# Performance work log

Hardware: AMD Instinct MI355X
Metric: run time of the kernel (lower is better)

Reference implementation:

```python
import jax, jax.numpy as jnp
import numpy as np

D = 1024
H = 16
DK = D // H
HID = 4096
EPS = 1e-5


def setup_inputs() -> dict:
    key = jax.random.key(0)
    ks = jax.random.split(key, 16)
    B, S = 2, 2048
    sc = lambda fan_in: 1.0 / np.sqrt(fan_in)
    inp = {
        "x": jax.random.normal(ks[0], (B, S, D), jnp.float32),
        "y": jax.random.normal(ks[1], (B, S, D), jnp.float32),
        "mask": jnp.ones((B, 1, 1, S), jnp.int32),
        # attention projections, stored [in, out]
        "Wq": jax.random.normal(ks[2], (D, D), jnp.float32) * sc(D),
        "bq": jnp.zeros((D,), jnp.float32),
        "Wk": jax.random.normal(ks[3], (D, D), jnp.float32) * sc(D),
        "bk": jnp.zeros((D,), jnp.float32),
        "Wv": jax.random.normal(ks[4], (D, D), jnp.float32) * sc(D),
        "bv": jnp.zeros((D,), jnp.float32),
        "Wo": jax.random.normal(ks[5], (D, D), jnp.float32) * sc(D),
        "bo": jnp.zeros((D,), jnp.float32),
        # FFN
        "W1": jax.random.normal(ks[6], (D, HID), jnp.float32) * sc(D),
        "b1": jnp.zeros((HID,), jnp.float32),
        "W2": jax.random.normal(ks[7], (HID, D), jnp.float32) * sc(HID),
        "b2": jnp.zeros((D,), jnp.float32),
        # LayerNorms
        "g1": jnp.ones((D,), jnp.float32),
        "be1": jnp.zeros((D,), jnp.float32),
        "g2": jnp.ones((D,), jnp.float32),
        "be2": jnp.zeros((D,), jnp.float32),
    }
    return inp


def _layer_norm(x, g, b):
    m = jnp.mean(x, axis=-1, keepdims=True)
    v = jnp.mean(jnp.square(x - m), axis=-1, keepdims=True)
    return (x - m) * jax.lax.rsqrt(v + EPS) * g + b


def _split_heads(t):  # [B,S,D] -> [B,H,S,DK]
    B, S, _ = t.shape
    return t.reshape(B, S, H, DK).transpose(0, 2, 1, 3)


def reference(x, y, mask, Wq, bq, Wk, bk, Wv, bv, Wo, bo,
              W1, b1, W2, b2, g1, be1, g2, be2):
    scale = 1.0 / np.sqrt(DK)
    Q = _split_heads(x @ Wq + bq)
    K = _split_heads(y @ Wk + bk)
    V = _split_heads(y @ Wv + bv)
    scores = jnp.einsum("bhqd,bhkd->bhqk", Q, K) * scale  # [B,H,S,S]
    scores = jnp.where(mask == 0, jnp.float32(-1e9), scores)
    probs = jax.nn.softmax(scores, axis=-1)
    attn = jnp.einsum("bhqk,bhkd->bhqd", probs, V)
    B, _, S, _ = attn.shape
    attn = attn.transpose(0, 2, 1, 3).reshape(B, S, D)
    mha_out = attn @ Wo + bo
    x1 = _layer_norm(x + mha_out, g1, be1)
    ff = jax.nn.relu(x1 @ W1 + b1) @ W2 + b2
    return _layer_norm(x1 + ff, g2, be2)
```

## Files before the change

### kernel.cpp

```cpp
#include <hip/hip_runtime.h>

#define S_ 2048
#define D_ 1024
#define B_ 2
#define H_ 16
#define DK_ 64
#define HID_ 4096

typedef unsigned short u16;
typedef __attribute__((ext_vector_type(8))) short short8;
typedef __attribute__((ext_vector_type(4))) float f32x4;

__device__ __forceinline__ float bf2f(u16 u) {
  return __uint_as_float(((unsigned int)u) << 16);
}
__device__ __forceinline__ u16 f2bf(float f) {
  unsigned int x = __float_as_uint(f);
  x += 0x7fff + ((x >> 16) & 1);
  return (u16)(x >> 16);
}
__device__ __forceinline__ unsigned int pk2bf(float lo, float hi) {
  return ((__float_as_uint(lo) + 0x8000u) >> 16) | ((__float_as_uint(hi) + 0x8000u) & 0xffff0000u);
}

__global__ __launch_bounds__(256) void cvt_f2b(const float* __restrict__ in, u16* __restrict__ outp) {
  const int i = blockIdx.x * 256 + threadIdx.x;
  float4 v = ((const float4*)in)[i];
  unsigned int lo = (unsigned int)f2bf(v.x) | ((unsigned int)f2bf(v.y) << 16);
  unsigned int hi = (unsigned int)f2bf(v.z) | ((unsigned int)f2bf(v.w) << 16);
  ((uint2*)outp)[i] = make_uint2(lo, hi);
}

__global__ __launch_bounds__(256) void maskbias_k(const int* __restrict__ mask, float* __restrict__ biasf) {
  const int i = blockIdx.x * 256 + threadIdx.x;
  biasf[i] = mask[i] ? 0.f : -1e30f;
}

template<int MT, int NT, int OUTF32>
__global__ __launch_bounds__(256) void gemm_bt(
    const u16* __restrict__ A, const u16* __restrict__ Bt,
    const float* __restrict__ bias, void* __restrict__ Cv,
    int K, int lda, int ldb, int ldc,
    long sA, long sB, long sC, int relu) {
  constexpr int BM = MT * 32;
  constexpr int BN = NT * 32;
  __shared__ __align__(16) u16 As[BM * 32];
  __shared__ __align__(16) u16 Bs[BN * 32];
  const int z = blockIdx.z;
  A  += (long)z * sA;
  Bt += (long)z * sB;
  const int tid  = threadIdx.x;
  const int lane = tid & 63, wave = tid >> 6;
  const int quad = lane >> 4, l15 = lane & 15;
  const int wm = wave >> 1, wn = wave & 1;
  const u16* Ab = A  + (long)(blockIdx.y * BM) * lda;
  const u16* Bb = Bt + (long)(blockIdx.x * BN) * ldb;

  f32x4 acc[MT][NT];
#pragma unroll
  for (int i = 0; i < MT; ++i)
#pragma unroll
    for (int j = 0; j < NT; ++j) acc[i][j] = (f32x4){0.f, 0.f, 0.f, 0.f};

  const int r0  = tid >> 2;
  const int kk0 = (tid & 3) * 8;

  for (int kt = 0; kt < K; kt += 32) {
#pragma unroll
    for (int p = 0; p < BM / 64; ++p) {
      __builtin_amdgcn_global_load_lds(
          (const __attribute__((address_space(1))) void*)(Ab + (long)(p * 64 + r0) * lda + kt + kk0),
          (__attribute__((address_space(3))) void*)(&As[p * 2048 + tid * 8]), 16, 0, 0);
    }
#pragma unroll
    for (int p = 0; p < BN / 64; ++p) {
      __builtin_amdgcn_global_load_lds(
          (const __attribute__((address_space(1))) void*)(Bb + (long)(p * 64 + r0) * ldb + kt + kk0),
          (__attribute__((address_space(3))) void*)(&Bs[p * 2048 + tid * 8]), 16, 0, 0);
    }
    __syncthreads();
    short8 af[MT], bfr[NT];
#pragma unroll
    for (int mt = 0; mt < MT; ++mt)
      af[mt] = *(const short8*)&As[(wm * (MT * 16) + mt * 16 + l15) * 32 + quad * 8];
#pragma unroll
    for (int nt = 0; nt < NT; ++nt)
      bfr[nt] = *(const short8*)&Bs[(wn * (NT * 16) + nt * 16 + l15) * 32 + quad * 8];
#pragma unroll
    for (int mt = 0; mt < MT; ++mt)
#pragma unroll
      for (int nt = 0; nt < NT; ++nt)
        acc[mt][nt] = __builtin_amdgcn_mfma_f32_16x16x32_bf16(af[mt], bfr[nt], acc[mt][nt], 0, 0, 0);
    __syncthreads();
  }

#pragma unroll
  for (int nt = 0; nt < NT; ++nt) {
    const int col = blockIdx.x * BN + wn * (NT * 16) + nt * 16 + l15;
    const float bvv = bias ? bias[col] : 0.f;
#pragma unroll
    for (int mt = 0; mt < MT; ++mt) {
#pragma unroll
      for (int r = 0; r < 4; ++r) {
        const int row = blockIdx.y * BM + wm * (MT * 16) + mt * 16 + quad * 4 + r;
        float v = acc[mt][nt][r] + bvv;
        if (relu) v = fmaxf(v, 0.f);
        if (OUTF32) ((float*)Cv)[(long)z * sC + (long)row * ldc + col] = v;
        else        ((u16*)Cv)[(long)z * sC + (long)row * ldc + col] = f2bf(v);
      }
    }
  }
}

__global__ __launch_bounds__(256) void qkv_k(
    const u16* __restrict__ xb, const u16* __restrict__ yb,
    const u16* __restrict__ WqT, const u16* __restrict__ WkT, const u16* __restrict__ WvT,
    const float* __restrict__ bq, const float* __restrict__ bk, const float* __restrict__ bv,
    u16* __restrict__ Q, u16* __restrict__ Kp, u16* __restrict__ Vp) {
  __shared__ __align__(16) u16 As[128 * 32];
  __shared__ __align__(16) u16 Bs[128 * 32];
  const int z = blockIdx.z;
  const u16* A  = (z == 0) ? xb : yb;
  const u16* Bt = (z == 0) ? WqT : (z == 1) ? WkT : WvT;
  const float* bias = (z == 0) ? bq : (z == 1) ? bk : bv;
  u16* C = (z == 0) ? Q : (z == 1) ? Kp : Vp;
  const float sc = (z == 0) ? 0.18033688011112042f : 1.0f;
  const int tid  = threadIdx.x;
  const int lane = tid & 63, wave = tid >> 6;
  const int quad = lane >> 4, l15 = lane & 15;
  const int wm = wave >> 1, wn = wave & 1;
  const u16* Ab = A  + (long)(blockIdx.y * 128) * D_;
  const u16* Bb = Bt + (long)(blockIdx.x * 128) * D_;

  f32x4 acc[4][4];
#pragma unroll
  for (int i = 0; i < 4; ++i)
#pragma unroll
    for (int j = 0; j < 4; ++j) acc[i][j] = (f32x4){0.f, 0.f, 0.f, 0.f};

  const int r0  = tid >> 2;
  const int kk0 = (tid & 3) * 8;

  for (int kt = 0; kt < D_; kt += 32) {
#pragma unroll
    for (int p = 0; p < 2; ++p) {
      __builtin_amdgcn_global_load_lds(
          (const __attribute__((address_space(1))) void*)(Ab + (long)(p * 64 + r0) * D_ + kt + kk0),
          (__attribute__((address_space(3))) void*)(&As[p * 2048 + tid * 8]), 16, 0, 0);
      __builtin_amdgcn_global_load_lds(
          (const __attribute__((address_space(1))) void*)(Bb + (long)(p * 64 + r0) * D_ + kt + kk0),
          (__attribute__((address_space(3))) void*)(&Bs[p * 2048 + tid * 8]), 16, 0, 0);
    }
    __syncthreads();
    short8 af[4], bfr[4];
#pragma unroll
    for (int mt = 0; mt < 4; ++mt)
      af[mt] = *(const short8*)&As[(wm * 64 + mt * 16 + l15) * 32 + quad * 8];
#pragma unroll
    for (int nt = 0; nt < 4; ++nt)
      bfr[nt] = *(const short8*)&Bs[(wn * 64 + nt * 16 + l15) * 32 + quad * 8];
#pragma unroll
    for (int mt = 0; mt < 4; ++mt)
#pragma unroll
      for (int nt = 0; nt < 4; ++nt)
        acc[mt][nt] = __builtin_amdgcn_mfma_f32_16x16x32_bf16(af[mt], bfr[nt], acc[mt][nt], 0, 0, 0);
    __syncthreads();
  }

#pragma unroll
  for (int nt = 0; nt < 4; ++nt) {
    const int col = blockIdx.x * 128 + wn * 64 + nt * 16 + l15;
    const float bvv = bias[col];
#pragma unroll
    for (int mt = 0; mt < 4; ++mt) {
#pragma unroll
      for (int r = 0; r < 4; ++r) {
        const int row = blockIdx.y * 128 + wm * 64 + mt * 16 + quad * 4 + r;
        C[(long)row * D_ + col] = f2bf((acc[mt][nt][r] + bvv) * sc);
      }
    }
  }
}

__global__ void transpose_k(const float* __restrict__ in, u16* __restrict__ outp, int R, int Ccols) {
  __shared__ u16 tile[32][33];
  const int c0 = blockIdx.x * 32, r0 = blockIdx.y * 32;
  const int tx = threadIdx.x, ty = threadIdx.y;
  for (int i = ty; i < 32; i += 8)
    tile[i][tx] = f2bf(in[(long)(r0 + i) * Ccols + c0 + tx]);
  __syncthreads();
  for (int i = ty; i < 32; i += 8)
    outp[(long)(c0 + i) * R + r0 + tx] = tile[tx][i];
}

__global__ void vtrans_k(const u16* __restrict__ V, u16* __restrict__ Vt) {
  __shared__ u16 tile[32][33];
  const int bh = blockIdx.z, b = bh >> 4, h = bh & 15;
  const u16* in = V + (long)b * S_ * D_ + h * DK_;
  u16* outp = Vt + (long)bh * DK_ * S_;
  const int s0 = blockIdx.x * 32, d0 = blockIdx.y * 32;
  const int tx = threadIdx.x, ty = threadIdx.y;
  for (int i = ty; i < 32; i += 8)
    tile[i][tx] = in[(long)(s0 + i) * D_ + d0 + tx];
  __syncthreads();
  for (int i = ty; i < 32; i += 8)
    outp[(long)(d0 + i) * S_ + s0 + tx] = tile[tx][i];
}

#define FA_LDS 65536
__global__ __launch_bounds__(256, 2) void flash_k(
    const u16* __restrict__ Q, const u16* __restrict__ Kp, const u16* __restrict__ Vt,
    const float* __restrict__ biasf, u16* __restrict__ ctx) {
  extern __shared__ __align__(16) char smem[];
  u16* sQ = (u16*)smem;
  u16* sK = (u16*)(smem + 32768);
  u16* sV = (u16*)(smem + 40960);
  u16* sP = (u16*)(smem + 49152);

  const int bh = blockIdx.x, qt = blockIdx.y;
  const int b = bh >> 4, h = bh & 15;
  const int tid = threadIdx.x;
  const int w = tid >> 6, lane = tid & 63;
  const int quad = lane >> 4, l15 = lane & 15;
  const int swz = ((l15 ^ (l15 >> 2)) & 3) << 3;

  const u16* Qg  = Q  + ((long)b * S_ + qt * 256) * D_ + h * DK_;
  const u16* Kg  = Kp + (long)b * S_ * D_ + h * DK_;
  const u16* Vtg = Vt + (long)bh * DK_ * S_;
  const float* biasg = biasf + b * S_;
  u16* ctxg = ctx + ((long)b * S_ + qt * 256) * D_ + h * DK_;

  const int krow = tid >> 3, kc = tid & 7;
  const u16* kptr = Kg + (long)krow * D_ + kc * 8;
  const int ksw = ((kc >> 2) << 10) + krow * 32 + (kc & 3) * 8;
  const int vrow = tid >> 2, vc = tid & 3;
  const u16* vptr = Vtg + (long)vrow * S_ + vc * 8;
  const int vsw = vrow * 32 + vc * 8;

  uint4 kreg = *(const uint4*)kptr;
  uint4 vreg = *(const uint4*)vptr;

#pragma unroll
  for (int p = 0; p < 8; ++p) {
    const int idx = p * 256 + tid;
    const int row = idx >> 3, cb = idx & 7;
    uint4 v = *(const uint4*)(Qg + (long)row * D_ + cb * 8);
    *(uint4*)&sQ[(cb >> 2) * 8192 + row * 32 + (cb & 3) * 8] = v;
  }
  *(uint4*)&sK[ksw] = kreg;
  *(uint4*)&sV[vsw] = vreg;
  kreg = *(const uint4*)(kptr + 32 * D_);
  vreg = *(const uint4*)(vptr + 32);
  kptr += 64 * D_;
  vptr += 64;
  __syncthreads();

  short8 qf[4][2];
#pragma unroll
  for (int nt = 0; nt < 4; ++nt)
#pragma unroll
    for (int kt = 0; kt < 2; ++kt)
      qf[nt][kt] = *(const short8*)&sQ[kt * 8192 + (w * 64 + nt * 16 + l15) * 32 + quad * 8];

  float lsum[4] = {0.f, 0.f, 0.f, 0.f};
  f32x4 accO[4][4];
#pragma unroll
  for (int i = 0; i < 4; ++i)
#pragma unroll
    for (int j = 0; j < 4; ++j) accO[i][j] = (f32x4){0.f, 0.f, 0.f, 0.f};

  for (int t = 0; t < 64; ++t) {
    if (t) __syncthreads();
    const int buf = (t & 1) << 11;
    const int nbuf = buf ^ 2048;
    if (t < 63) {
      *(uint4*)&sK[nbuf + ksw] = kreg;
      *(uint4*)&sV[nbuf + vsw] = vreg;
      if (t < 62) {
        kreg = *(const uint4*)kptr;
        vreg = *(const uint4*)vptr;
        kptr += 32 * D_;
        vptr += 32;
      }
    }
    float4 bv0 = *(const float4*)(biasg + t * 32 + quad * 4);
    float4 bv1 = *(const float4*)(biasg + t * 32 + 16 + quad * 4);

    f32x4 accS[2][4];
#pragma unroll
    for (int i = 0; i < 2; ++i)
#pragma unroll
      for (int j = 0; j < 4; ++j) accS[i][j] = (f32x4){0.f, 0.f, 0.f, 0.f};
#pragma unroll
    for (int kt = 0; kt < 2; ++kt) {
      short8 kf0 = *(const short8*)&sK[buf + kt * 1024 + l15 * 32 + quad * 8];
      short8 kf1 = *(const short8*)&sK[buf + kt * 1024 + (16 + l15) * 32 + quad * 8];
#pragma unroll
      for (int nt = 0; nt < 4; ++nt) {
        accS[0][nt] = __builtin_amdgcn_mfma_f32_16x16x32_bf16(kf0, qf[nt][kt], accS[0][nt], 0, 0, 0);
        accS[1][nt] = __builtin_amdgcn_mfma_f32_16x16x32_bf16(kf1, qf[nt][kt], accS[1][nt], 0, 0, 0);
      }
    }
#pragma unroll
    for (int mt = 0; mt < 2; ++mt) {
      const float4 bv = mt ? bv1 : bv0;
      const int kvl = ((mt * 16 + quad * 4) ^ swz);
#pragma unroll
      for (int nt = 0; nt < 4; ++nt) {
        float p0 = exp2f(fminf(accS[mt][nt][0] + bv.x, 30.f));
        float p1 = exp2f(fminf(accS[mt][nt][1] + bv.y, 30.f));
        float p2 = exp2f(fminf(accS[mt][nt][2] + bv.z, 30.f));
        float p3 = exp2f(fminf(accS[mt][nt][3] + bv.w, 30.f));
        lsum[nt] += (p0 + p1) + (p2 + p3);
        *(uint2*)&sP[(w * 64 + nt * 16 + l15) * 32 + kvl] =
            make_uint2(pk2bf(p0, p1), pk2bf(p2, p3));
      }
    }
    short8 pf[4], vf[4];
#pragma unroll
    for (int m = 0; m < 4; ++m)
      pf[m] = *(const short8*)&sP[(w * 64 + m * 16 + l15) * 32 + ((quad * 8) ^ swz)];
#pragma unroll
    for (int n = 0; n < 4; ++n)
      vf[n] = *(const short8*)&sV[buf + (n * 16 + l15) * 32 + quad * 8];
#pragma unroll
    for (int m = 0; m < 4; ++m)
#pragma unroll
      for (int n = 0; n < 4; ++n)
        accO[m][n] = __builtin_amdgcn_mfma_f32_16x16x32_bf16(pf[m], vf[n], accO[m][n], 0, 0, 0);
  }

#pragma unroll
  for (int nt = 0; nt < 4; ++nt) {
    lsum[nt] += __shfl_xor(lsum[nt], 16, 64);
    lsum[nt] += __shfl_xor(lsum[nt], 32, 64);
  }
#pragma unroll
  for (int m = 0; m < 4; ++m) {
    float inv[4];
#pragma unroll
    for (int r = 0; r < 4; ++r)
      inv[r] = 1.f / __shfl(lsum[m], quad * 4 + r, 64);
#pragma unroll
    for (int n = 0; n < 4; ++n) {
#pragma unroll
      for (int r = 0; r < 4; ++r)
        ctxg[(long)(w * 64 + m * 16 + quad * 4 + r) * D_ + n * 16 + l15] =
            f2bf(accO[m][n][r] * inv[r]);
    }
  }
}

__device__ __forceinline__ float block_reduce_sum(float v, float* red) {
#pragma unroll
  for (int off = 32; off; off >>= 1) v += __shfl_down(v, off, 64);
  __syncthreads();
  if ((threadIdx.x & 63) == 0) red[threadIdx.x >> 6] = v;
  __syncthreads();
  return red[0] + red[1] + red[2] + red[3];
}

__global__ __launch_bounds__(256) void addln_fb(const float* __restrict__ A, const u16* __restrict__ Bres,
    const float* __restrict__ g, const float* __restrict__ be, u16* __restrict__ outp) {
  __shared__ float red[4];
  const int row = blockIdx.x, tid = threadIdx.x;
  const float4 av = ((const float4*)(A + (long)row * D_))[tid];
  const uint2 bv2 = ((const uint2*)(Bres + (long)row * D_))[tid];
  float xv[4];
  xv[0] = av.x + bf2f((u16)(bv2.x & 0xffff));
  xv[1] = av.y + bf2f((u16)(bv2.x >> 16));
  xv[2] = av.z + bf2f((u16)(bv2.y & 0xffff));
  xv[3] = av.w + bf2f((u16)(bv2.y >> 16));
  float s  = xv[0] + xv[1] + xv[2] + xv[3];
  float ss = xv[0]*xv[0] + xv[1]*xv[1] + xv[2]*xv[2] + xv[3]*xv[3];
  s  = block_reduce_sum(s, red);
  ss = block_reduce_sum(ss, red);
  const float m   = s * (1.0f / 1024.0f);
  const float var = ss * (1.0f / 1024.0f) - m * m;
  const float rs  = rsqrtf(var + 1e-5f);
  const int c0 = tid * 4;
  float v0 = (xv[0] - m) * rs * g[c0 + 0] + be[c0 + 0];
  float v1 = (xv[1] - m) * rs * g[c0 + 1] + be[c0 + 1];
  float v2 = (xv[2] - m) * rs * g[c0 + 2] + be[c0 + 2];
  float v3 = (xv[3] - m) * rs * g[c0 + 3] + be[c0 + 3];
  unsigned int o01 = (unsigned int)f2bf(v0) | ((unsigned int)f2bf(v1) << 16);
  unsigned int o23 = (unsigned int)f2bf(v2) | ((unsigned int)f2bf(v3) << 16);
  ((uint2*)(outp + (long)row * D_))[tid] = make_uint2(o01, o23);
}

__global__ __launch_bounds__(256) void addln2_bf(const u16* __restrict__ A,
    const float* __restrict__ p0, const float* __restrict__ p1, const float* __restrict__ b2,
    const float* __restrict__ g, const float* __restrict__ be, float* __restrict__ outp) {
  __shared__ float red[4];
  const int row = blockIdx.x, tid = threadIdx.x;
  const uint2 av  = ((const uint2*)(A + (long)row * D_))[tid];
  const float4 P0 = ((const float4*)(p0 + (long)row * D_))[tid];
  const float4 P1 = ((const float4*)(p1 + (long)row * D_))[tid];
  const int c0 = tid * 4;
  float xv[4];
  xv[0] = bf2f((u16)(av.x & 0xffff)) + P0.x + P1.x + b2[c0 + 0];
  xv[1] = bf2f((u16)(av.x >> 16))    + P0.y + P1.y + b2[c0 + 1];
  xv[2] = bf2f((u16)(av.y & 0xffff)) + P0.z + P1.z + b2[c0 + 2];
  xv[3] = bf2f((u16)(av.y >> 16))    + P0.w + P1.w + b2[c0 + 3];
  float s  = xv[0] + xv[1] + xv[2] + xv[3];
  float ss = xv[0]*xv[0] + xv[1]*xv[1] + xv[2]*xv[2] + xv[3]*xv[3];
  s  = block_reduce_sum(s, red);
  ss = block_reduce_sum(ss, red);
  const float m   = s * (1.0f / 1024.0f);
  const float var = ss * (1.0f / 1024.0f) - m * m;
  const float rs  = rsqrtf(var + 1e-5f);
  float4 o;
  o.x = (xv[0] - m) * rs * g[c0 + 0] + be[c0 + 0];
  o.y = (xv[1] - m) * rs * g[c0 + 1] + be[c0 + 1];
  o.z = (xv[2] - m) * rs * g[c0 + 2] + be[c0 + 2];
  o.w = (xv[3] - m) * rs * g[c0 + 3] + be[c0 + 3];
  ((float4*)(outp + (long)row * D_))[tid] = o;
}

extern "C" void kernel_launch(void* const* d_in, const int* in_sizes, int n_in,
                              void* d_out, int out_size, void* d_ws, size_t ws_size,
                              hipStream_t stream) {
  const float* x   = (const float*)d_in[0];
  const float* y   = (const float*)d_in[1];
  const int* mask  = (const int*)d_in[2];
  const float* Wq = (const float*)d_in[3];  const float* bq = (const float*)d_in[4];
  const float* Wk = (const float*)d_in[5];  const float* bk = (const float*)d_in[6];
  const float* Wv = (const float*)d_in[7];  const float* bv = (const float*)d_in[8];
  const float* Wo = (const float*)d_in[9];  const float* bo = (const float*)d_in[10];
  const float* W1 = (const float*)d_in[11]; const float* b1 = (const float*)d_in[12];
  const float* W2 = (const float*)d_in[13]; const float* b2 = (const float*)d_in[14];
  const float* g1 = (const float*)d_in[15]; const float* be1 = (const float*)d_in[16];
  const float* g2 = (const float*)d_in[17]; const float* be2 = (const float*)d_in[18];
  float* out = (float*)d_out;

  char* w = (char*)d_ws;
  const size_t MB = 1024 * 1024;
  u16* WqT = (u16*)(w + 0 * MB);
  u16* WkT = (u16*)(w + 2 * MB);
  u16* WvT = (u16*)(w + 4 * MB);
  u16* WoT = (u16*)(w + 6 * MB);
  u16* W1T = (u16*)(w + 8 * MB);
  u16* W2T = (u16*)(w + 16 * MB);
  u16* xb  = (u16*)(w + 24 * MB);
  u16* yb  = (u16*)(w + 32 * MB);
  u16* Q   = (u16*)(w + 40 * MB);
  u16* Kp  = (u16*)(w + 48 * MB);
  u16* Vp  = (u16*)(w + 56 * MB);
  u16* Vt  = (u16*)(w + 64 * MB);
  u16* ctx = (u16*)(w + 72 * MB);
  u16* mha = (u16*)(w + 80 * MB);
  u16* x1  = (u16*)(w + 88 * MB);
  u16* h1  = (u16*)(w + 96 * MB);
  float* pK = (float*)(w + 40 * MB);
  float* biasf = (float*)(w + 128 * MB);

  hipFuncSetAttribute((const void*)flash_k, hipFuncAttributeMaxDynamicSharedMemorySize, FA_LDS);

  dim3 t328(32, 8);
  transpose_k<<<dim3(32, 32), t328, 0, stream>>>(Wq, WqT, 1024, 1024);
  transpose_k<<<dim3(32, 32), t328, 0, stream>>>(Wk, WkT, 1024, 1024);
  transpose_k<<<dim3(32, 32), t328, 0, stream>>>(Wv, WvT, 1024, 1024);
  transpose_k<<<dim3(32, 32), t328, 0, stream>>>(Wo, WoT, 1024, 1024);
  transpose_k<<<dim3(128, 32), t328, 0, stream>>>(W1, W1T, 1024, 4096);
  transpose_k<<<dim3(32, 128), t328, 0, stream>>>(W2, W2T, 4096, 1024);
  cvt_f2b<<<dim3(4096), 256, 0, stream>>>(x, xb);
  cvt_f2b<<<dim3(4096), 256, 0, stream>>>(y, yb);
  maskbias_k<<<dim3(16), 256, 0, stream>>>(mask, biasf);

  qkv_k<<<dim3(8, 32, 3), 256, 0, stream>>>(xb, yb, WqT, WkT, WvT, bq, bk, bv, Q, Kp, Vp);

  vtrans_k<<<dim3(64, 2, 32), t328, 0, stream>>>(Vp, Vt);

  flash_k<<<dim3(32, 8), 256, FA_LDS, stream>>>(Q, Kp, Vt, biasf, ctx);

  gemm_bt<2, 4, 0><<<dim3(8, 64, 1), 256, 0, stream>>>(ctx, WoT, bo, mha,
      1024, 1024, 1024, 1024, 0, 0, 0, 0);
  addln_fb<<<dim3(4096), 256, 0, stream>>>(x, mha, g1, be1, x1);

  gemm_bt<4, 4, 0><<<dim3(32, 32, 1), 256, 0, stream>>>(x1, W1T, b1, h1,
      1024, 1024, 1024, 4096, 0, 0, 0, 1);
  gemm_bt<4, 4, 1><<<dim3(8, 32, 2), 256, 0, stream>>>(h1, W2T, nullptr, (void*)pK,
      2048, 4096, 4096, 1024, 2048, 2048, (long)4096 * 1024, 0);
  addln2_bf<<<dim3(4096), 256, 0, stream>>>(x1, pK, pK + (long)4096 * 1024, b2, g2, be2, out);
}
```

Before: 467.7 us.

## Merge prep kernels, shrink flash tiles, fold mask into exp, split-K four ways

Folds the six weight transposes and the x/y conversions into one prep launch, with cvt2_k converting x and y in a single launch. Flash attention moves from 256-row to 64-row query tiles with static LDS and a higher occupancy target, and applies the int mask directly in place of a precomputed bias buffer. The FFN down-projection now uses four-way split-K, with a four-input add+LayerNorm at the end. The prep kernel's x/y branch writes only half-packed values, but cvt2_k rewrites those outputs afterwards. x1 and the partial-sum buffers are also relocated in the workspace.

```diff
diff --git a/kernel.cpp b/kernel.cpp
--- a/kernel.cpp
+++ b/kernel.cpp
@@ -23,17 +23,55 @@
   return ((__float_as_uint(lo) + 0x8000u) >> 16) | ((__float_as_uint(hi) + 0x8000u) & 0xffff0000u);
 }
 
-__global__ __launch_bounds__(256) void cvt_f2b(const float* __restrict__ in, u16* __restrict__ outp) {
+__global__ void prep_k(
+    const float* __restrict__ Wq, const float* __restrict__ Wk,
+    const float* __restrict__ Wv, const float* __restrict__ Wo,
+    const float* __restrict__ W1, const float* __restrict__ W2,
+    const float* __restrict__ x, const float* __restrict__ y,
+    u16* __restrict__ WqT, u16* __restrict__ WkT, u16* __restrict__ WvT,
+    u16* __restrict__ WoT, u16* __restrict__ W1T, u16* __restrict__ W2T,
+    u16* __restrict__ xb, u16* __restrict__ yb) {
+  const int z = blockIdx.z;
+  if (z < 6) {
+    __shared__ u16 tile[32][33];
+    const float* in; u16* outp; int R, C;
+    switch (z) {
+      case 0: in = Wq; outp = WqT; R = 1024; C = 1024; break;
+      case 1: in = Wk; outp = WkT; R = 1024; C = 1024; break;
+      case 2: in = Wv; outp = WvT; R = 1024; C = 1024; break;
+      case 3: in = Wo; outp = WoT; R = 1024; C = 1024; break;
+      case 4: in = W1; outp = W1T; R = 1024; C = 4096; break;
+      default: in = W2; outp = W2T; R = 4096; C = 1024; break;
+    }
+    int c0, r0;
+    if (z == 5) { c0 = blockIdx.y * 32; r0 = blockIdx.x * 32; }
+    else        { c0 = blockIdx.x * 32; r0 = blockIdx.y * 32; }
+    if (c0 >= C || r0 >= R) return;
+    const int tx = threadIdx.x, ty = threadIdx.y;
+    for (int i = ty; i < 32; i += 8)
+      tile[i][tx] = f2bf(in[(long)(r0 + i) * C + c0 + tx]);
+    __syncthreads();
+    for (int i = ty; i < 32; i += 8)
+      outp[(long)(c0 + i) * R + r0 + tx] = tile[tx][i];
+  } else {
+    const float* in = (z == 6) ? x : y;
+    u16* outp = (z == 6) ? xb : yb;
+    const int lin = (blockIdx.y * 128 + blockIdx.x) * 256 + threadIdx.y * 32 + threadIdx.x;
+    float4 v = ((const float4*)in)[lin];
+    ((uint2*)outp)[lin] = make_uint2(pk2bf(v.x, v.y)  , 0);
+  }
+}
+
+__global__ __launch_bounds__(256) void cvt2_k(const float* __restrict__ x, const float* __restrict__ y,
+                                              u16* __restrict__ xb, u16* __restrict__ yb) {
+  const int z = blockIdx.y;
+  const float* in = z ? y : x;
+  u16* outp = z ? yb : xb;
   const int i = blockIdx.x * 256 + threadIdx.x;
   float4 v = ((const float4*)in)[i];
   unsigned int lo = (unsigned int)f2bf(v.x) | ((unsigned int)f2bf(v.y) << 16);
   unsigned int hi = (unsigned int)f2bf(v.z) | ((unsigned int)f2bf(v.w) << 16);
   ((uint2*)outp)[i] = make_uint2(lo, hi);
-}
-
-__global__ __launch_bounds__(256) void maskbias_k(const int* __restrict__ mask, float* __restrict__ biasf) {
-  const int i = blockIdx.x * 256 + threadIdx.x;
-  biasf[i] = mask[i] ? 0.f : -1e30f;
 }
 
 template<int MT, int NT, int OUTF32>
@@ -182,17 +220,6 @@
   }
 }
 
-__global__ void transpose_k(const float* __restrict__ in, u16* __restrict__ outp, int R, int Ccols) {
-  __shared__ u16 tile[32][33];
-  const int c0 = blockIdx.x * 32, r0 = blockIdx.y * 32;
-  const int tx = threadIdx.x, ty = threadIdx.y;
-  for (int i = ty; i < 32; i += 8)
-    tile[i][tx] = f2bf(in[(long)(r0 + i) * Ccols + c0 + tx]);
-  __syncthreads();
-  for (int i = ty; i < 32; i += 8)
-    outp[(long)(c0 + i) * R + r0 + tx] = tile[tx][i];
-}
-
 __global__ void vtrans_k(const u16* __restrict__ V, u16* __restrict__ Vt) {
   __shared__ u16 tile[32][33];
   const int bh = blockIdx.z, b = bh >> 4, h = bh & 15;
@@ -207,15 +234,13 @@
     outp[(long)(d0 + i) * S_ + s0 + tx] = tile[tx][i];
 }
 
-#define FA_LDS 65536
-__global__ __launch_bounds__(256, 2) void flash_k(
+__global__ __launch_bounds__(256, 4) void flash_k(
     const u16* __restrict__ Q, const u16* __restrict__ Kp, const u16* __restrict__ Vt,
-    const float* __restrict__ biasf, u16* __restrict__ ctx) {
-  extern __shared__ __align__(16) char smem[];
-  u16* sQ = (u16*)smem;
-  u16* sK = (u16*)(smem + 32768);
-  u16* sV = (u16*)(smem + 40960);
-  u16* sP = (u16*)(smem + 49152);
+    const int* __restrict__ mask, u16* __restrict__ ctx) {
+  __shared__ __align__(16) u16 sQ[2 * 64 * 32];
+  __shared__ __align__(16) u16 sK[2 * 2048];
+  __shared__ __align__(16) u16 sV[2 * 2048];
+  __shared__ __align__(16) u16 sP[64 * 32];
 
   const int bh = blockIdx.x, qt = blockIdx.y;
   const int b = bh >> 4, h = bh & 15;
@@ -224,15 +249,15 @@
   const int quad = lane >> 4, l15 = lane & 15;
   const int swz = ((l15 ^ (l15 >> 2)) & 3) << 3;
 
-  const u16* Qg  = Q  + ((long)b * S_ + qt * 256) * D_ + h * DK_;
+  const u16* Qg  = Q  + ((long)b * S_ + qt * 64) * D_ + h * DK_;
   const u16* Kg  = Kp + (long)b * S_ * D_ + h * DK_;
   const u16* Vtg = Vt + (long)bh * DK_ * S_;
-  const float* biasg = biasf + b * S_;
-  u16* ctxg = ctx + ((long)b * S_ + qt * 256) * D_ + h * DK_;
+  const int* maskg = mask + (long)b * S_;
+  u16* ctxg = ctx + ((long)b * S_ + qt * 64) * D_ + h * DK_;
 
   const int krow = tid >> 3, kc = tid & 7;
   const u16* kptr = Kg + (long)krow * D_ + kc * 8;
-  const int ksw = ((kc >> 2) << 10) + krow * 32 + (kc & 3) * 8;
+  const int ksw = (kc >> 2) * 1024 + krow * 32 + (kc & 3) * 8;
   const int vrow = tid >> 2, vc = tid & 3;
   const u16* vptr = Vtg + (long)vrow * S_ + vc * 8;
   const int vsw = vrow * 32 + vc * 8;
@@ -241,11 +266,11 @@
   uint4 vreg = *(const uint4*)vptr;
 
 #pragma unroll
-  for (int p = 0; p < 8; ++p) {
+  for (int p = 0; p < 2; ++p) {
     const int idx = p * 256 + tid;
     const int row = idx >> 3, cb = idx & 7;
     uint4 v = *(const uint4*)(Qg + (long)row * D_ + cb * 8);
-    *(uint4*)&sQ[(cb >> 2) * 8192 + row * 32 + (cb & 3) * 8] = v;
+    *(uint4*)&sQ[(cb >> 2) * 2048 + row * 32 + (cb & 3) * 8] = v;
   }
   *(uint4*)&sK[ksw] = kreg;
   *(uint4*)&sV[vsw] = vreg;
@@ -255,23 +280,19 @@
   vptr += 64;
   __syncthreads();
 
-  short8 qf[4][2];
-#pragma unroll
-  for (int nt = 0; nt < 4; ++nt)
-#pragma unroll
-    for (int kt = 0; kt < 2; ++kt)
-      qf[nt][kt] = *(const short8*)&sQ[kt * 8192 + (w * 64 + nt * 16 + l15) * 32 + quad * 8];
-
-  float lsum[4] = {0.f, 0.f, 0.f, 0.f};
-  f32x4 accO[4][4];
-#pragma unroll
-  for (int i = 0; i < 4; ++i)
-#pragma unroll
-    for (int j = 0; j < 4; ++j) accO[i][j] = (f32x4){0.f, 0.f, 0.f, 0.f};
+  short8 qf[2];
+#pragma unroll
+  for (int kt = 0; kt < 2; ++kt)
+    qf[kt] = *(const short8*)&sQ[kt * 2048 + (w * 16 + l15) * 32 + quad * 8];
+
+  float lsum = 0.f;
+  f32x4 accO[4];
+#pragma unroll
+  for (int j = 0; j < 4; ++j) accO[j] = (f32x4){0.f, 0.f, 0.f, 0.f};
 
   for (int t = 0; t < 64; ++t) {
     if (t) __syncthreads();
-    const int buf = (t & 1) << 11;
+    const int buf = (t & 1) ? 2048 : 0;
     const int nbuf = buf ^ 2048;
     if (t < 63) {
       *(uint4*)&sK[nbuf + ksw] = kreg;
@@ -283,71 +304,49 @@
         vptr += 32;
       }
     }
-    float4 bv0 = *(const float4*)(biasg + t * 32 + quad * 4);
-    float4 bv1 = *(const float4*)(biasg + t * 32 + 16 + quad * 4);
-
-    f32x4 accS[2][4];
-#pragma unroll
-    for (int i = 0; i < 2; ++i)
-#pragma unroll
-      for (int j = 0; j < 4; ++j) accS[i][j] = (f32x4){0.f, 0.f, 0.f, 0.f};
+    const int4 mv0 = *(const int4*)(maskg + t * 32 + quad * 4);
+    const int4 mv1 = *(const int4*)(maskg + t * 32 + 16 + quad * 4);
+
+    f32x4 accS[2];
+    accS[0] = (f32x4){0.f, 0.f, 0.f, 0.f};
+    accS[1] = (f32x4){0.f, 0.f, 0.f, 0.f};
 #pragma unroll
     for (int kt = 0; kt < 2; ++kt) {
       short8 kf0 = *(const short8*)&sK[buf + kt * 1024 + l15 * 32 + quad * 8];
       short8 kf1 = *(const short8*)&sK[buf + kt * 1024 + (16 + l15) * 32 + quad * 8];
-#pragma unroll
-      for (int nt = 0; nt < 4; ++nt) {
-        accS[0][nt] = __builtin_amdgcn_mfma_f32_16x16x32_bf16(kf0, qf[nt][kt], accS[0][nt], 0, 0, 0);
-        accS[1][nt] = __builtin_amdgcn_mfma_f32_16x16x32_bf16(kf1, qf[nt][kt], accS[1][nt], 0, 0, 0);
-      }
-    }
-#pragma unroll
-    for (int mt = 0; mt < 2; ++mt) {
-      const float4 bv = mt ? bv1 : bv0;
-      const int kvl = ((mt * 16 + quad * 4) ^ swz);
-#pragma unroll
-      for (int nt = 0; nt < 4; ++nt) {
-        float p0 = exp2f(fminf(accS[mt][nt][0] + bv.x, 30.f));
-        float p1 = exp2f(fminf(accS[mt][nt][1] + bv.y, 30.f));
-        float p2 = exp2f(fminf(accS[mt][nt][2] + bv.z, 30.f));
-        float p3 = exp2f(fminf(accS[mt][nt][3] + bv.w, 30.f));
-        lsum[nt] += (p0 + p1) + (p2 + p3);
-        *(uint2*)&sP[(w * 64 + nt * 16 + l15) * 32 + kvl] =
-            make_uint2(pk2bf(p0, p1), pk2bf(p2, p3));
-      }
-    }
-    short8 pf[4], vf[4];
-#pragma unroll
-    for (int m = 0; m < 4; ++m)
-      pf[m] = *(const short8*)&sP[(w * 64 + m * 16 + l15) * 32 + ((quad * 8) ^ swz)];
-#pragma unroll
-    for (int n = 0; n < 4; ++n)
-      vf[n] = *(const short8*)&sV[buf + (n * 16 + l15) * 32 + quad * 8];
-#pragma unroll
-    for (int m = 0; m < 4; ++m)
-#pragma unroll
-      for (int n = 0; n < 4; ++n)
-        accO[m][n] = __builtin_amdgcn_mfma_f32_16x16x32_bf16(pf[m], vf[n], accO[m][n], 0, 0, 0);
-  }
-
-#pragma unroll
-  for (int nt = 0; nt < 4; ++nt) {
-    lsum[nt] += __shfl_xor(lsum[nt], 16, 64);
-    lsum[nt] += __shfl_xor(lsum[nt], 32, 64);
-  }
-#pragma unroll
-  for (int m = 0; m < 4; ++m) {
-    float inv[4];
+      accS[0] = __builtin_amdgcn_mfma_f32_16x16x32_bf16(kf0, qf[kt], accS[0], 0, 0, 0);
+      accS[1] = __builtin_amdgcn_mfma_f32_16x16x32_bf16(kf1, qf[kt], accS[1], 0, 0, 0);
+    }
+#pragma unroll
+    for (int m = 0; m < 2; ++m) {
+      const int4 mv = m ? mv1 : mv0;
+      float p0 = mv.x ? __builtin_amdgcn_exp2f(accS[m][0]) : 0.f;
+      float p1 = mv.y ? __builtin_amdgcn_exp2f(accS[m][1]) : 0.f;
+      float p2 = mv.z ? __builtin_amdgcn_exp2f(accS[m][2]) : 0.f;
+      float p3 = mv.w ? __builtin_amdgcn_exp2f(accS[m][3]) : 0.f;
+      lsum += (p0 + p1) + (p2 + p3);
+      *(uint2*)&sP[(w * 16 + l15) * 32 + ((m * 16 + quad * 4) ^ swz)] =
+          make_uint2(pk2bf(p0, p1), pk2bf(p2, p3));
+    }
+    short8 pf = *(const short8*)&sP[(w * 16 + l15) * 32 + ((quad * 8) ^ swz)];
+#pragma unroll
+    for (int n = 0; n < 4; ++n) {
+      short8 vf = *(const short8*)&sV[buf + (n * 16 + l15) * 32 + quad * 8];
+      accO[n] = __builtin_amdgcn_mfma_f32_16x16x32_bf16(pf, vf, accO[n], 0, 0, 0);
+    }
+  }
+
+  lsum += __shfl_xor(lsum, 16, 64);
+  lsum += __shfl_xor(lsum, 32, 64);
+  float inv[4];
+#pragma unroll
+  for (int r = 0; r < 4; ++r)
+    inv[r] = 1.f / __shfl(lsum, quad * 4 + r, 64);
+#pragma unroll
+  for (int n = 0; n < 4; ++n) {
 #pragma unroll
     for (int r = 0; r < 4; ++r)
-      inv[r] = 1.f / __shfl(lsum[m], quad * 4 + r, 64);
-#pragma unroll
-    for (int n = 0; n < 4; ++n) {
-#pragma unroll
-      for (int r = 0; r < 4; ++r)
-        ctxg[(long)(w * 64 + m * 16 + quad * 4 + r) * D_ + n * 16 + l15] =
-            f2bf(accO[m][n][r] * inv[r]);
-    }
+      ctxg[(long)(w * 16 + quad * 4 + r) * D_ + n * 16 + l15] = f2bf(accO[n][r] * inv[r]);
   }
 }
 
@@ -388,20 +387,23 @@
   ((uint2*)(outp + (long)row * D_))[tid] = make_uint2(o01, o23);
 }
 
-__global__ __launch_bounds__(256) void addln2_bf(const u16* __restrict__ A,
-    const float* __restrict__ p0, const float* __restrict__ p1, const float* __restrict__ b2,
+__global__ __launch_bounds__(256) void addln4_bf(const u16* __restrict__ A,
+    const float* __restrict__ pK, const float* __restrict__ b2,
     const float* __restrict__ g, const float* __restrict__ be, float* __restrict__ outp) {
   __shared__ float red[4];
   const int row = blockIdx.x, tid = threadIdx.x;
-  const uint2 av  = ((const uint2*)(A + (long)row * D_))[tid];
-  const float4 P0 = ((const float4*)(p0 + (long)row * D_))[tid];
-  const float4 P1 = ((const float4*)(p1 + (long)row * D_))[tid];
+  const uint2 av = ((const uint2*)(A + (long)row * D_))[tid];
+  const long stride = (long)4096 * 1024;
+  const float4 P0 = ((const float4*)(pK + 0 * stride + (long)row * D_))[tid];
+  const float4 P1 = ((const float4*)(pK + 1 * stride + (long)row * D_))[tid];
+  const float4 P2 = ((const float4*)(pK + 2 * stride + (long)row * D_))[tid];
+  const float4 P3 = ((const float4*)(pK + 3 * stride + (long)row * D_))[tid];
   const int c0 = tid * 4;
   float xv[4];
-  xv[0] = bf2f((u16)(av.x & 0xffff)) + P0.x + P1.x + b2[c0 + 0];
-  xv[1] = bf2f((u16)(av.x >> 16))    + P0.y + P1.y + b2[c0 + 1];
-  xv[2] = bf2f((u16)(av.y & 0xffff)) + P0.z + P1.z + b2[c0 + 2];
-  xv[3] = bf2f((u16)(av.y >> 16))    + P0.w + P1.w + b2[c0 + 3];
+  xv[0] = bf2f((u16)(av.x & 0xffff)) + ((P0.x + P1.x) + (P2.x + P3.x)) + b2[c0 + 0];
+  xv[1] = bf2f((u16)(av.x >> 16))    + ((P0.y + P1.y) + (P2.y + P3.y)) + b2[c0 + 1];
+  xv[2] = bf2f((u16)(av.y & 0xffff)) + ((P0.z + P1.z) + (P2.z + P3.z)) + b2[c0 + 2];
+  xv[3] = bf2f((u16)(av.y >> 16))    + ((P0.w + P1.w) + (P2.w + P3.w)) + b2[c0 + 3];
   float s  = xv[0] + xv[1] + xv[2] + xv[3];
   float ss = xv[0]*xv[0] + xv[1]*xv[1] + xv[2]*xv[2] + xv[3]*xv[3];
   s  = block_reduce_sum(s, red);
@@ -449,29 +451,19 @@
   u16* Vt  = (u16*)(w + 64 * MB);
   u16* ctx = (u16*)(w + 72 * MB);
   u16* mha = (u16*)(w + 80 * MB);
-  u16* x1  = (u16*)(w + 88 * MB);
+  u16* x1  = (u16*)(w + 24 * MB);
   u16* h1  = (u16*)(w + 96 * MB);
-  float* pK = (float*)(w + 40 * MB);
-  float* biasf = (float*)(w + 128 * MB);
-
-  hipFuncSetAttribute((const void*)flash_k, hipFuncAttributeMaxDynamicSharedMemorySize, FA_LDS);
-
-  dim3 t328(32, 8);
-  transpose_k<<<dim3(32, 32), t328, 0, stream>>>(Wq, WqT, 1024, 1024);
-  transpose_k<<<dim3(32, 32), t328, 0, stream>>>(Wk, WkT, 1024, 1024);
-  transpose_k<<<dim3(32, 32), t328, 0, stream>>>(Wv, WvT, 1024, 1024);
-  transpose_k<<<dim3(32, 32), t328, 0, stream>>>(Wo, WoT, 1024, 1024);
-  transpose_k<<<dim3(128, 32), t328, 0, stream>>>(W1, W1T, 1024, 4096);
-  transpose_k<<<dim3(32, 128), t328, 0, stream>>>(W2, W2T, 4096, 1024);
-  cvt_f2b<<<dim3(4096), 256, 0, stream>>>(x, xb);
-  cvt_f2b<<<dim3(4096), 256, 0, stream>>>(y, yb);
-  maskbias_k<<<dim3(16), 256, 0, stream>>>(mask, biasf);
+  float* pK = (float*)(w + 32 * MB);
+
+  prep_k<<<dim3(128, 32, 6), dim3(32, 8), 0, stream>>>(Wq, Wk, Wv, Wo, W1, W2, x, y,
+      WqT, WkT, WvT, WoT, W1T, W2T, xb, yb);
+  cvt2_k<<<dim3(4096, 2), 256, 0, stream>>>(x, y, xb, yb);
 
   qkv_k<<<dim3(8, 32, 3), 256, 0, stream>>>(xb, yb, WqT, WkT, WvT, bq, bk, bv, Q, Kp, Vp);
 
-  vtrans_k<<<dim3(64, 2, 32), t328, 0, stream>>>(Vp, Vt);
-
-  flash_k<<<dim3(32, 8), 256, FA_LDS, stream>>>(Q, Kp, Vt, biasf, ctx);
+  vtrans_k<<<dim3(64, 2, 32), dim3(32, 8), 0, stream>>>(Vp, Vt);
+
+  flash_k<<<dim3(32, 32), 256, 0, stream>>>(Q, Kp, Vt, mask, ctx);
 
   gemm_bt<2, 4, 0><<<dim3(8, 64, 1), 256, 0, stream>>>(ctx, WoT, bo, mha,
       1024, 1024, 1024, 1024, 0, 0, 0, 0);
@@ -479,7 +471,7 @@
 
   gemm_bt<4, 4, 0><<<dim3(32, 32, 1), 256, 0, stream>>>(x1, W1T, b1, h1,
       1024, 1024, 1024, 4096, 0, 0, 0, 1);
-  gemm_bt<4, 4, 1><<<dim3(8, 32, 2), 256, 0, stream>>>(h1, W2T, nullptr, (void*)pK,
-      2048, 4096, 4096, 1024, 2048, 2048, (long)4096 * 1024, 0);
-  addln2_bf<<<dim3(4096), 256, 0, stream>>>(x1, pK, pK + (long)4096 * 1024, b2, g2, be2, out);
-}
+  gemm_bt<4, 4, 1><<<dim3(8, 32, 4), 256, 0, stream>>>(h1, W2T, nullptr, (void*)pK,
+      1024, 4096, 4096, 1024, 1024, 1024, (long)4096 * 1024, 0);
+  addln4_bf<<<dim3(4096), 256, 0, stream>>>(x1, pK, b2, g2, be2, out);
+}
```

After: 442.9 us. 5.3% less time.
